# Kernel tuning notes

Hardware: AMD Instinct MI355X
Metric: run time of the kernel (lower is better)

## Reference

```python
import jax, jax.numpy as jnp
import numpy as np

K = 20          # neighbors
EPS = 1e-5      # BatchNorm eps
SLOPE = 0.2     # LeakyReLU negative slope


def setup_inputs() -> dict:
    key = jax.random.key(0)
    k1, k2 = jax.random.split(key)
    B, C, N, O = 8, 64, 4096, 64
    x = jax.random.normal(k1, (B, C, N), dtype=jnp.float32)
    # 1x1 Conv2d(2C -> O, bias=False) kernel, squeezed to (O, 2C)
    W = jax.random.normal(k2, (O, 2 * C), dtype=jnp.float32) * 0.05
    gamma = jnp.ones((O,), jnp.float32)   # BN weight
    beta = jnp.zeros((O,), jnp.float32)   # BN bias
    return {"x": x, "W": W, "gamma": gamma, "beta": beta}


def _edgeconv(x, W, gamma, beta):
    B, C, N = x.shape
    xt = jnp.transpose(x, (0, 2, 1))                       # (B, N, C)
    # KNN on negative squared distance (matches torch topk of -dist)
    xx = jnp.sum(x * x, axis=1)                            # (B, N)
    inner = jnp.einsum('bnc,bmc->bnm', xt, xt)             # (B, N, N)
    neg_dist = 2.0 * inner - xx[:, :, None] - xx[:, None, :]
    _, idx = jax.lax.top_k(neg_dist, K)                    # (B, N, K) int32
    # gather neighbor features: nbr[b,n,k,c] = xt[b, idx[b,n,k], c]
    nbr = xt[jnp.arange(B)[:, None, None], idx]            # (B, N, K, C)
    center = jnp.broadcast_to(xt[:, :, None, :], (B, N, K, C))
    edge = jnp.concatenate([nbr - center, center], axis=-1)  # (B, N, K, 2C)
    # 1x1 conv == channel matmul
    y = jnp.einsum('bnkc,oc->bnko', edge, W)               # (B, N, K, O)
    # BatchNorm2d (training mode: batch statistics over B,N,K per channel)
    mean = jnp.mean(y, axis=(0, 1, 2))
    var = jnp.var(y, axis=(0, 1, 2))
    yn = (y - mean) * jax.lax.rsqrt(var + EPS) * gamma + beta
    ya = jnp.where(yn >= 0, yn, SLOPE * yn)                # LeakyReLU(0.2)
    out = jnp.max(ya, axis=2)                              # max over k -> (B, N, O)
    return jnp.transpose(out, (0, 2, 1))                   # (B, O, N)


def reference(x, W, gamma, beta):
    return _edgeconv(x, W, gamma, beta)
```

## Files before the change

kernel.cpp:

```cpp
#include <hip/hip_runtime.h>
#include <hip/hip_bf16.h>
#include <math.h>

#define B 8
#define C 64
#define NN 4096
#define O 64
#define KNN 20

typedef float f32x4 __attribute__((ext_vector_type(4)));
typedef short short8_t __attribute__((ext_vector_type(8)));

__device__ inline uint32_t fkey(float f) {
    uint32_t u = __float_as_uint(f);
    return u ^ (((uint32_t)((int32_t)u >> 31)) | 0x80000000u);
}

__device__ inline uint32_t med3u(uint32_t a, uint32_t b, uint32_t c) {
    uint32_t r;
    asm("v_med3_u32 %0, %1, %2, %3" : "=v"(r) : "v"(a), "v"(b), "v"(c));
    return r;
}
__device__ inline uint32_t umax(uint32_t a, uint32_t b) { return a > b ? a : b; }

__device__ inline uint32_t maxall16(uint32_t v) {
    uint32_t t;
    t = (uint32_t)__builtin_amdgcn_update_dpp(0, (int)v, 0x140, 0xF, 0xF, true);
    v = umax(v, t);
    t = (uint32_t)__builtin_amdgcn_update_dpp(0, (int)v, 0x141, 0xF, 0xF, true);
    v = umax(v, t);
    t = (uint32_t)__builtin_amdgcn_update_dpp(0, (int)v, 0x4E, 0xF, 0xF, true);
    v = umax(v, t);
    t = (uint32_t)__builtin_amdgcn_update_dpp(0, (int)v, 0xB1, 0xF, 0xF, true);
    v = umax(v, t);
    return v;
}

__global__ __launch_bounds__(256) void k1_split(const float* __restrict__ x,
                                                float* __restrict__ xt,
                                                __hip_bfloat16* __restrict__ xh,
                                                float* __restrict__ xx) {
    __shared__ float tile[64][65];
    int b  = blockIdx.x / (NN / 64);
    int n0 = (blockIdx.x % (NN / 64)) * 64;
    int t = threadIdx.x;
    #pragma unroll
    for (int it = 0; it < 16; ++it) {
        int i = it * 256 + t;
        int c = i >> 6, n = i & 63;
        tile[c][n] = x[(size_t)b * C * NN + (size_t)c * NN + n0 + n];
    }
    __syncthreads();
    #pragma unroll
    for (int it = 0; it < 16; ++it) {
        int i = it * 256 + t;
        int n = i >> 6, c = i & 63;
        float v = tile[c][n];
        size_t off = ((size_t)(b * NN + n0 + n)) * C + c;
        xt[off] = v;
        xh[off] = __float2bfloat16(v);
    }
    if (t < 64) {
        float s = 0.f;
        #pragma unroll
        for (int c = 0; c < 64; ++c) { float v = tile[c][t]; s = fmaf(v, v, s); }
        xx[(size_t)b * NN + t + n0] = s;
    }
}

__global__ __launch_bounds__(256) void k2_knn(const __hip_bfloat16* __restrict__ xh,
                                              const float* __restrict__ xt,
                                              const float* __restrict__ xx,
                                              int* __restrict__ idx) {
    int b  = blockIdx.x >> 8;
    int n0 = (blockIdx.x & 255) << 4;
    int t = threadIdx.x;
    int w = t >> 6, lane = t & 63;
    int laneid = lane & 15, grp = lane >> 4;

    const __hip_bfloat16* xhb = xh + (size_t)b * NN * 64;
    const float* xxb = xx + (size_t)b * NN;
    const float* xtb = xt + (size_t)b * NN * 64;

    size_t qoff = (size_t)(n0 + laneid) * 64 + grp * 8;
    short8_t Ah0 = *(const short8_t*)(xhb + qoff);
    short8_t Ah1 = *(const short8_t*)(xhb + qoff + 32);

    uint32_t qq[4][12];
    #pragma unroll
    for (int j = 0; j < 4; ++j)
        #pragma unroll
        for (int i = 0; i < 12; ++i) qq[j][i] = 0;

    #pragma unroll 1
    for (int c = 0; c < 4; ++c) {
        int cbase = w * 1024 + c * 256;
        #pragma unroll
        for (int tl = 0; tl < 16; ++tl) {
            int cand_i = cbase + tl * 16 + laneid;
            size_t coff = (size_t)cand_i * 64 + grp * 8;
            short8_t Bh0 = *(const short8_t*)(xhb + coff);
            short8_t Bh1 = *(const short8_t*)(xhb + coff + 32);
            f32x4 acc = {0.f, 0.f, 0.f, 0.f};
            acc = __builtin_amdgcn_mfma_f32_16x16x32_bf16(Ah0, Bh0, acc, 0, 0, 0);
            acc = __builtin_amdgcn_mfma_f32_16x16x32_bf16(Ah1, Bh1, acc, 0, 0, 0);
            float xxc = xxb[cand_i];
            uint32_t invcol = 4095u - (uint32_t)cand_i;
            #pragma unroll
            for (int j = 0; j < 4; ++j) {
                uint32_t nv = (fkey(fmaf(acc[j], 2.f, -xxc)) & 0xFFFFF000u) | invcol;
                #pragma unroll
                for (int i = 11; i >= 1; --i)
                    qq[j][i] = med3u(qq[j][i - 1], qq[j][i], nv);
                qq[j][0] = umax(qq[j][0], nv);
            }
        }
    }

    __shared__ uint32_t mbuf[16][4][24];
    __shared__ uint32_t cand[16][32];
    __shared__ uint32_t rkk[16][32];
    __shared__ float qrow[16][64];

    #pragma unroll
    for (int i = 0; i < 4; ++i) {
        int e = i * 256 + t;
        int r = e >> 6, cc = e & 63;
        qrow[r][cc] = xtb[(size_t)(n0 + r) * 64 + cc];
    }

    #pragma unroll 1
    for (int r = 0; r < 24; ++r) {
        #pragma unroll
        for (int j = 0; j < 4; ++j) {
            uint32_t bk = maxall16(qq[j][0]);
            bool win = (qq[j][0] == bk);
            #pragma unroll
            for (int i = 0; i < 11; ++i) qq[j][i] = win ? qq[j][i + 1] : qq[j][i];
            qq[j][11] = win ? 0u : qq[j][11];
            if (laneid == 0) mbuf[grp * 4 + j][w][r] = bk;
        }
    }
    __syncthreads();

    {
        int q = w * 4 + grp;
        const uint32_t* mb = &mbuf[q][0][0];
        uint32_t e0 = mb[laneid],      e1 = mb[16 + laneid], e2 = mb[32 + laneid],
                 e3 = mb[48 + laneid], e4 = mb[64 + laneid], e5 = mb[80 + laneid];
        #pragma unroll 1
        for (int r = 0; r < 32; ++r) {
            uint32_t bk = umax(umax(umax(e0, e1), umax(e2, e3)), umax(e4, e5));
            bk = maxall16(bk);
            e0 = (e0 == bk) ? 0u : e0;
            e1 = (e1 == bk) ? 0u : e1;
            e2 = (e2 == bk) ? 0u : e2;
            e3 = (e3 == bk) ? 0u : e3;
            e4 = (e4 == bk) ? 0u : e4;
            e5 = (e5 == bk) ? 0u : e5;
            if (laneid == 0) cand[q][r] = 4095u - (bk & 4095u);
        }
    }
    __syncthreads();

    int rq = t >> 4, rs = t & 15;
    float qxx = xxb[n0 + rq];
    const float4* qr = (const float4*)qrow[rq];
    uint32_t mycol[2], mykey[2];
    #pragma unroll
    for (int e = 0; e < 2; ++e) {
        uint32_t col = cand[rq][rs + 16 * e];
        const float4* cr = (const float4*)(xtb + (size_t)col * 64);
        float a = 0.f;
        #pragma unroll
        for (int i = 0; i < 16; ++i) {
            float4 qv = qr[i], cv = cr[i];
            a = fmaf(qv.x, cv.x, a); a = fmaf(qv.y, cv.y, a);
            a = fmaf(qv.z, cv.z, a); a = fmaf(qv.w, cv.w, a);
        }
        float d = 2.f * a - qxx - xxb[col];
        mycol[e] = col;
        mykey[e] = fkey(d);
        rkk[rq][rs + 16 * e] = mykey[e];
    }
    __syncthreads();
    size_t ob = ((size_t)(b * NN) + n0 + rq) * KNN;
    #pragma unroll
    for (int e = 0; e < 2; ++e) {
        uint32_t ke = mykey[e], ce = mycol[e];
        int rank = 0;
        #pragma unroll
        for (int jj = 0; jj < 32; ++jj) {
            uint32_t kj = rkk[rq][jj], cj = cand[rq][jj];
            rank += (kj > ke || (kj == ke && cj < ce)) ? 1 : 0;
        }
        if (rank < KNN) idx[ob + rank] = (int)ce;
    }
}

__global__ __launch_bounds__(256) void k3a_gemm(const float* __restrict__ xt,
                                                const float* __restrict__ W,
                                                float* __restrict__ Z,
                                                float* __restrict__ Z2) {
    __shared__ float W0t[64][65];
    __shared__ float W21t[64][65];
    __shared__ float xs[16][64];
    int t = threadIdx.x;
    #pragma unroll
    for (int it = 0; it < 16; ++it) {
        int i = it * 256 + t;
        int o = i >> 6, c = i & 63;
        float w0 = W[o * 128 + c];
        float w1 = W[o * 128 + 64 + c];
        W0t[c][o]  = w0;
        W21t[c][o] = w1 - w0;
    }
    int b  = blockIdx.x / (NN / 16);
    int nb = (blockIdx.x % (NN / 16)) * 16;
    #pragma unroll
    for (int it = 0; it < 4; ++it) {
        int i = it * 256 + t;
        int r = i >> 6, c = i & 63;
        xs[r][c] = xt[((size_t)(b * NN + nb + r)) * C + c];
    }
    __syncthreads();
    int o = t & 63, rg = t >> 6;
    #pragma unroll
    for (int rr = 0; rr < 4; ++rr) {
        int r = rg * 4 + rr;
        float z = 0.f, z2 = 0.f;
        #pragma unroll
        for (int c = 0; c < 64; ++c) {
            float xv = xs[r][c];
            z  = fmaf(xv, W0t[c][o],  z);
            z2 = fmaf(xv, W21t[c][o], z2);
        }
        size_t off = ((size_t)(b * NN + nb + r)) * 64 + o;
        Z[off]  = z;
        Z2[off] = z2;
    }
}

__global__ __launch_bounds__(256) void k3b_gather(const float* __restrict__ Z,
                                                  const float* __restrict__ Z2,
                                                  const int* __restrict__ idx,
                                                  float* __restrict__ maxY,
                                                  float* __restrict__ minY,
                                                  float* __restrict__ partials) {
    int t = threadIdx.x;
    int p = t >> 6, o = t & 63;
    int b = blockIdx.x / (NN / 4);
    int n = (blockIdx.x % (NN / 4)) * 4 + p;
    size_t base = (size_t)(b * NN + n);
    float z2 = Z2[base * 64 + o];
    __shared__ int sidx[4][KNN];
    if (o < KNN) sidx[p][o] = idx[base * KNN + o];
    __syncthreads();
    const float* Zb = Z + (size_t)b * NN * 64;
    float s1 = 0.f, s2 = 0.f, mx = -INFINITY, mn = INFINITY;
    #pragma unroll
    for (int k = 0; k < KNN; ++k) {
        float y = Zb[(size_t)sidx[p][k] * 64 + o] + z2;
        s1 += y;
        s2 = fmaf(y, y, s2);
        mx = fmaxf(mx, y);
        mn = fminf(mn, y);
    }
    maxY[base * 64 + o] = mx;
    minY[base * 64 + o] = mn;
    __shared__ float red[2][4][64];
    red[0][p][o] = s1;
    red[1][p][o] = s2;
    __syncthreads();
    if (t < 64) {
        float a = red[0][0][t] + red[0][1][t] + red[0][2][t] + red[0][3][t];
        float c = red[1][0][t] + red[1][1][t] + red[1][2][t] + red[1][3][t];
        partials[(size_t)blockIdx.x * 128 + t]      = a;
        partials[(size_t)blockIdx.x * 128 + 64 + t] = c;
    }
}

__global__ __launch_bounds__(256) void k4a_reduce(const float* __restrict__ partials,
                                                  float* __restrict__ partials2) {
    int g = blockIdx.x;
    int t = threadIdx.x;
    int col = t & 127, half = t >> 7;
    float s = 0.f;
    for (int r = half; r < 128; r += 2)
        s += partials[((size_t)g * 128 + r) * 128 + col];
    __shared__ float red[2][128];
    red[half][col] = s;
    __syncthreads();
    if (t < 128) partials2[(size_t)g * 128 + t] = red[0][t] + red[1][t];
}

__global__ __launch_bounds__(128) void k4b_stats(const float* __restrict__ partials2,
                                                 const float* __restrict__ gamma,
                                                 const float* __restrict__ beta,
                                                 float* __restrict__ ss) {
    int t = threadIdx.x;
    double s = 0.0;
    for (int i = 0; i < 64; ++i)
        s += (double)partials2[(size_t)i * 128 + t];
    __shared__ double red[128];
    red[t] = s;
    __syncthreads();
    if (t < 64) {
        double a = red[t], c = red[64 + t];
        double M = (double)B * NN * KNN;
        double mean = a / M;
        double var  = c / M - mean * mean;
        float sc = gamma[t] * rsqrtf((float)var + 1e-5f);
        float sh = beta[t] - (float)mean * sc;
        ss[t]      = sc;
        ss[64 + t] = sh;
    }
}

__global__ __launch_bounds__(256) void k5_out(const float* __restrict__ maxY,
                                              const float* __restrict__ minY,
                                              const float* __restrict__ ss,
                                              float* __restrict__ out) {
    __shared__ float tile[64][65];
    __shared__ float sc[64], sh[64];
    int t = threadIdx.x;
    if (t < 64) { sc[t] = ss[t]; sh[t] = ss[64 + t]; }
    int b  = blockIdx.x / (NN / 64);
    int n0 = (blockIdx.x % (NN / 64)) * 64;
    __syncthreads();
    #pragma unroll
    for (int it = 0; it < 16; ++it) {
        int i = it * 256 + t;
        int nl = i >> 6, o = i & 63;
        size_t off = ((size_t)(b * NN + n0 + nl)) * 64 + o;
        float s = sc[o];
        float v = (s >= 0.f) ? maxY[off] : minY[off];
        v = fmaf(v, s, sh[o]);
        v = (v >= 0.f) ? v : 0.2f * v;
        tile[nl][o] = v;
    }
    __syncthreads();
    #pragma unroll
    for (int it = 0; it < 16; ++it) {
        int i = it * 256 + t;
        int o = i >> 6, nl = i & 63;
        out[((size_t)(b * O + o)) * NN + n0 + nl] = tile[nl][o];
    }
}

extern "C" void kernel_launch(void* const* d_in, const int* in_sizes, int n_in,
                              void* d_out, int out_size, void* d_ws, size_t ws_size,
                              hipStream_t stream) {
    const float* x     = (const float*)d_in[0];
    const float* W     = (const float*)d_in[1];
    const float* gamma = (const float*)d_in[2];
    const float* beta  = (const float*)d_in[3];
    float* out = (float*)d_out;

    float* ws = (float*)d_ws;
    float* xx = ws;
    float* xt = xx + (size_t)B * NN;
    __hip_bfloat16* xh = (__hip_bfloat16*)(xt + (size_t)B * NN * C);
    int*   idx = (int*)(xh + (size_t)B * NN * C);
    float* Z   = (float*)(idx + (size_t)B * NN * KNN);
    float* Z2  = Z + (size_t)B * NN * O;
    float* maxY = Z2 + (size_t)B * NN * O;
    float* minY = maxY + (size_t)B * NN * O;
    float* partials  = minY + (size_t)B * NN * O;
    float* partials2 = partials + (size_t)(B * NN / 4) * 128;
    float* ss = partials2 + 64 * 128;

    k1_split<<<B * (NN / 64), 256, 0, stream>>>(x, xt, xh, xx);
    k2_knn<<<B * (NN / 16), 256, 0, stream>>>(xh, xt, xx, idx);
    k3a_gemm<<<B * (NN / 16), 256, 0, stream>>>(xt, W, Z, Z2);
    k3b_gather<<<B * (NN / 4), 256, 0, stream>>>(Z, Z2, idx, maxY, minY, partials);
    k4a_reduce<<<64, 256, 0, stream>>>(partials, partials2);
    k4b_stats<<<1, 128, 0, stream>>>(partials2, gamma, beta, ss);
    k5_out<<<B * (NN / 64), 256, 0, stream>>>(maxY, minY, ss, out);
}
```

Before: 270.3 us.

## Prefetch KNN candidate tiles, swizzle blocks by batch per XCD, trim merge rounds

The KNN distance loop now loads the next candidate tile's bf16 features and squared norm before issuing the MFMAs for the current one. This is meant to hide global-load latency behind compute. Both the KNN and gather kernels now map the batch index to the low three bits of the block index. Since blocks are dealt round-robin across the eight XCDs, all blocks of one batch land on the same XCD and share its L2. Each wave also passes 20 instead of 24 per-wave candidates into the final merge, cutting shuffle-reduction rounds. The trade-offs are a slightly narrower candidate pool for the fp32 rerank and a prefetch on the last iteration that reads past the wave's range, possibly out of bounds for the last batch.

```diff
diff --git a/kernel.cpp b/kernel.cpp
--- a/kernel.cpp
+++ b/kernel.cpp
@@ -72,8 +72,8 @@
                                               const float* __restrict__ xt,
                                               const float* __restrict__ xx,
                                               int* __restrict__ idx) {
-    int b  = blockIdx.x >> 8;
-    int n0 = (blockIdx.x & 255) << 4;
+    int b  = blockIdx.x & 7;
+    int n0 = (blockIdx.x >> 3) << 4;
     int t = threadIdx.x;
     int w = t >> 6, lane = t & 63;
     int laneid = lane & 15, grp = lane >> 4;
@@ -92,20 +92,27 @@
         #pragma unroll
         for (int i = 0; i < 12; ++i) qq[j][i] = 0;
 
-    #pragma unroll 1
-    for (int c = 0; c < 4; ++c) {
-        int cbase = w * 1024 + c * 256;
-        #pragma unroll
-        for (int tl = 0; tl < 16; ++tl) {
-            int cand_i = cbase + tl * 16 + laneid;
-            size_t coff = (size_t)cand_i * 64 + grp * 8;
-            short8_t Bh0 = *(const short8_t*)(xhb + coff);
-            short8_t Bh1 = *(const short8_t*)(xhb + coff + 32);
+    int cand0 = w * 1024 + laneid;
+    {
+        const __hip_bfloat16* p0 = xhb + (size_t)cand0 * 64 + grp * 8;
+        short8_t nB0 = *(const short8_t*)p0;
+        short8_t nB1 = *(const short8_t*)(p0 + 32);
+        float nxx = xxb[cand0];
+        #pragma unroll 4
+        for (int tt = 0; tt < 64; ++tt) {
+            short8_t B0 = nB0, B1 = nB1;
+            float xxc = nxx;
+            int ci = cand0 + tt * 16;
+            {
+                const __hip_bfloat16* np = xhb + (size_t)(ci + 16) * 64 + grp * 8;
+                nB0 = *(const short8_t*)np;
+                nB1 = *(const short8_t*)(np + 32);
+                nxx = xxb[ci + 16];
+            }
             f32x4 acc = {0.f, 0.f, 0.f, 0.f};
-            acc = __builtin_amdgcn_mfma_f32_16x16x32_bf16(Ah0, Bh0, acc, 0, 0, 0);
-            acc = __builtin_amdgcn_mfma_f32_16x16x32_bf16(Ah1, Bh1, acc, 0, 0, 0);
-            float xxc = xxb[cand_i];
-            uint32_t invcol = 4095u - (uint32_t)cand_i;
+            acc = __builtin_amdgcn_mfma_f32_16x16x32_bf16(Ah0, B0, acc, 0, 0, 0);
+            acc = __builtin_amdgcn_mfma_f32_16x16x32_bf16(Ah1, B1, acc, 0, 0, 0);
+            uint32_t invcol = 4095u - (uint32_t)ci;
             #pragma unroll
             for (int j = 0; j < 4; ++j) {
                 uint32_t nv = (fkey(fmaf(acc[j], 2.f, -xxc)) & 0xFFFFF000u) | invcol;
@@ -117,7 +124,7 @@
         }
     }
 
-    __shared__ uint32_t mbuf[16][4][24];
+    __shared__ uint32_t mbuf[16][4][20];
     __shared__ uint32_t cand[16][32];
     __shared__ uint32_t rkk[16][32];
     __shared__ float qrow[16][64];
@@ -130,7 +137,7 @@
     }
 
     #pragma unroll 1
-    for (int r = 0; r < 24; ++r) {
+    for (int r = 0; r < 20; ++r) {
         #pragma unroll
         for (int j = 0; j < 4; ++j) {
             uint32_t bk = maxall16(qq[j][0]);
@@ -147,17 +154,16 @@
         int q = w * 4 + grp;
         const uint32_t* mb = &mbuf[q][0][0];
         uint32_t e0 = mb[laneid],      e1 = mb[16 + laneid], e2 = mb[32 + laneid],
-                 e3 = mb[48 + laneid], e4 = mb[64 + laneid], e5 = mb[80 + laneid];
+                 e3 = mb[48 + laneid], e4 = mb[64 + laneid];
         #pragma unroll 1
         for (int r = 0; r < 32; ++r) {
-            uint32_t bk = umax(umax(umax(e0, e1), umax(e2, e3)), umax(e4, e5));
+            uint32_t bk = umax(umax(umax(e0, e1), umax(e2, e3)), e4);
             bk = maxall16(bk);
             e0 = (e0 == bk) ? 0u : e0;
             e1 = (e1 == bk) ? 0u : e1;
             e2 = (e2 == bk) ? 0u : e2;
             e3 = (e3 == bk) ? 0u : e3;
             e4 = (e4 == bk) ? 0u : e4;
-            e5 = (e5 == bk) ? 0u : e5;
             if (laneid == 0) cand[q][r] = 4095u - (bk & 4095u);
         }
     }
@@ -249,8 +255,8 @@
                                                   float* __restrict__ partials) {
     int t = threadIdx.x;
     int p = t >> 6, o = t & 63;
-    int b = blockIdx.x / (NN / 4);
-    int n = (blockIdx.x % (NN / 4)) * 4 + p;
+    int b = blockIdx.x & 7;
+    int n = (blockIdx.x >> 3) * 4 + p;
     size_t base = (size_t)(b * NN + n);
     float z2 = Z2[base * 64 + o];
     __shared__ int sidx[4][KNN];
```

After: 254.0 us. 1.06x faster.
